# Kernel optimization log

Hardware: AMD Instinct MI355X
Metric: run time of the kernel (lower is better)

The kernel has to match this reference:

```python
import jax, jax.numpy as jnp
import numpy as np

QUANT_BITS = 8


def fake_quant(x, bits=QUANT_BITS):
    """Asymmetric signed per-tensor quantize->dequantize (GlobalMinMaxObserver)."""
    qmin = -(2 ** (bits - 1))
    qmax = 2 ** (bits - 1) - 1
    mn = jnp.minimum(jnp.min(x), 0.0)
    mx = jnp.maximum(jnp.max(x), 0.0)
    scale = jnp.maximum((mx - mn) / (qmax - qmin), 1e-8)
    zp = jnp.clip(jnp.round(qmin - mn / scale), qmin, qmax)
    q = jnp.clip(jnp.round(x / scale) + zp, qmin, qmax)
    return (q - zp) * scale


def hardsigmoid(x):
    return jnp.clip(x / 6.0 + 0.5, 0.0, 1.0)


def hardtanh(x):
    return jnp.clip(x, -1.0, 1.0)


def setup_inputs() -> dict:
    key = jax.random.key(0)
    ks = jax.random.split(key, 11)
    B, W, I, H = 16384, 32, 64, 64
    s = 1.0 / np.sqrt(I + H)
    return {
        "inputs": jax.random.normal(ks[0], (B, W, I), jnp.float32),
        "h_prev": jax.random.normal(ks[1], (B, W, H), jnp.float32),
        "c_prev": jax.random.normal(ks[2], (B, W, H), jnp.float32),
        "W_i": jax.random.normal(ks[3], (H, I + H), jnp.float32) * s,
        "b_i": jax.random.normal(ks[4], (H,), jnp.float32) * s,
        "W_f": jax.random.normal(ks[5], (H, I + H), jnp.float32) * s,
        "b_f": jax.random.normal(ks[6], (H,), jnp.float32) * s,
        "W_o": jax.random.normal(ks[7], (H, I + H), jnp.float32) * s,
        "b_o": jax.random.normal(ks[8], (H,), jnp.float32) * s,
        "W_c": jax.random.normal(ks[9], (H, I + H), jnp.float32) * s,
        "b_c": jax.random.normal(ks[10], (H,), jnp.float32) * s,
    }


def reference(inputs, h_prev, c_prev, W_i, b_i, W_f, b_f, W_o, b_o, W_c, b_c):
    # fake-quant every tensor as the module's QParams/observers do
    x = fake_quant(inputs)
    h = fake_quant(h_prev)
    c = fake_quant(c_prev)
    cat = fake_quant(jnp.concatenate([x, h], axis=-1))  # [B, W, I+H]

    def gate(Wg, bg):
        return fake_quant(jnp.einsum("bwk,hk->bwh", cat, fake_quant(Wg)) + fake_quant(bg))

    i_g = fake_quant(hardsigmoid(gate(W_i, b_i)))
    f_g = fake_quant(hardsigmoid(gate(W_f, b_f)))
    o_g = fake_quant(hardsigmoid(gate(W_o, b_o)))
    c_g = fake_quant(hardtanh(gate(W_c, b_c)))

    fc = fake_quant(f_g * c)
    ic = fake_quant(i_g * c_g)
    c_next = fake_quant(fc + ic)
    c_next_tanh = fake_quant(hardtanh(c_next))
    h_next = fake_quant(o_g * c_next_tanh)
    return h_next, c_next
```

## Files before the change

### kernel.cpp

```cpp
#include <hip/hip_runtime.h>
#include <stdint.h>

#define NE    33554432
#define MROWS 524288

typedef __attribute__((ext_vector_type(8))) short short8;
typedef __attribute__((ext_vector_type(4))) float f32x4;
typedef unsigned short ushort_t;
typedef unsigned char uchar_t;

__device__ __forceinline__ unsigned fenc(float f){
  unsigned u=__float_as_uint(f); return (u&0x80000000u)?~u:(u|0x80000000u);
}
__device__ __forceinline__ float fdec(unsigned u){
  return __uint_as_float((u&0x80000000u)?(u&0x7fffffffu):~u);
}
__device__ __forceinline__ void obs(float mn,float mx,float&s,float&zp){
  mn=fminf(mn,0.f); mx=fmaxf(mx,0.f);
  s=fmaxf((mx-mn)/255.0f,1e-8f);
  zp=fminf(fmaxf(rintf(-128.0f-mn/s),-128.f),127.f);
}
__device__ __forceinline__ float qof(float x,float s,float zp){
  return fminf(fmaxf(rintf(x/s)+zp,-128.f),127.f);
}
__device__ __forceinline__ float fqv(float x,float s,float zp){
  return (qof(x,s,zp)-zp)*s;
}
__device__ __forceinline__ void wred(float&mn,float&mx){
  #pragma unroll
  for(int o=32;o;o>>=1){mn=fminf(mn,__shfl_xor(mn,o));mx=fmaxf(mx,__shfl_xor(mx,o));}
}


__global__ void k0_init(unsigned* U){
  int t=threadIdx.x;
  if(t<11){U[2*t]=0xFFFFFFFFu;U[2*t+1]=0u;}
}

__global__ __launch_bounds__(256) void k1_minmax(const float* __restrict__ x,
    const float* __restrict__ h,const float* __restrict__ c,unsigned* U){
  __shared__ float red[8];
  int t=blockIdx.x*256+threadIdx.x, stride=gridDim.x*256;
  int w=threadIdx.x>>6,l=threadIdx.x&63;
  const float4* ps[3]={(const float4*)x,(const float4*)h,(const float4*)c};
  for(int q=0;q<3;q++){
    float mn=3.4e38f,mx=-3.4e38f;
    const float4* p=ps[q];
    for(int e=t;e<NE/4;e+=stride){
      float4 v=p[e];
      mn=fminf(mn,fminf(fminf(v.x,v.y),fminf(v.z,v.w)));
      mx=fmaxf(mx,fmaxf(fmaxf(v.x,v.y),fmaxf(v.z,v.w)));
    }
    wred(mn,mx);
    if(l==0){red[w]=mn;red[4+w]=mx;}
    __syncthreads();
    if(threadIdx.x==0){
      float bmn=fminf(fminf(red[0],red[1]),fminf(red[2],red[3]));
      float bmx=fmaxf(fmaxf(red[4],red[5]),fmaxf(red[6],red[7]));
      atomicMin(&U[2*q],fenc(bmn)); atomicMax(&U[2*q+1],fenc(bmx));
    }
    __syncthreads();
  }
}

__global__ __launch_bounds__(256) void k2_prep(const float* Wi,const float* bi,
    const float* Wf,const float* bfv,const float* Wo,const float* bo,
    const float* Wcg,const float* bcg,
    const unsigned* U,float* S,ushort_t* Wc,float* bq){
  __shared__ float smn[256],smx[256],sP[4];
  int t=threadIdx.x;
  if(t==0){
    float xmn=fdec(U[0]),xmx=fdec(U[1]),hmn=fdec(U[2]),hmx=fdec(U[3]),cmn=fdec(U[4]),cmx=fdec(U[5]);
    float sx,zx,sh,zh,sc,zc;
    obs(xmn,xmx,sx,zx);obs(hmn,hmx,sh,zh);obs(cmn,cmx,sc,zc);
    S[0]=sx;S[1]=zx;S[2]=sh;S[3]=zh;S[4]=sc;S[5]=zc;
    float cmn2=fminf(fqv(xmn,sx,zx),fqv(hmn,sh,zh));
    float cmx2=fmaxf(fqv(xmx,sx,zx),fqv(hmx,sh,zh));
    float scat,zcat;obs(cmn2,cmx2,scat,zcat);S[6]=scat;S[7]=zcat;
  }
  const float* Wp[4]={Wi,Wf,Wo,Wcg};
  const float* bp[4]={bi,bfv,bo,bcg};
  for(int g=0;g<4;g++){
    float mn=3.4e38f,mx=-3.4e38f;
    for(int i=t;i<8192;i+=256){float v=Wp[g][i];mn=fminf(mn,v);mx=fmaxf(mx,v);}
    smn[t]=mn;smx[t]=mx;__syncthreads();
    for(int ss=128;ss;ss>>=1){
      if(t<ss){smn[t]=fminf(smn[t],smn[t+ss]);smx[t]=fmaxf(smx[t],smx[t+ss]);}
      __syncthreads();
    }
    if(t==0){
      float s_,z_;obs(smn[0],smx[0],s_,z_);
      S[8+2*g]=s_;S[9+2*g]=z_;sP[0]=s_;sP[1]=z_;
      float bmn=3.4e38f,bmx=-3.4e38f;
      for(int i=0;i<64;i++){float v=bp[g][i];bmn=fminf(bmn,v);bmx=fmaxf(bmx,v);}
      float sb,zb;obs(bmn,bmx,sb,zb);sP[2]=sb;sP[3]=zb;
    }
    __syncthreads();
    float s_=sP[0],z_=sP[1],sb=sP[2],zb=sP[3];
    for(int i=t;i<8192;i+=256){
      float cv=qof(Wp[g][i],s_,z_)-z_;
      Wc[g*8192+i]=(ushort_t)(__float_as_uint(cv)>>16);
    }
    if(t<64) bq[g*64+t]=fqv(bp[g][t],sb,zb);
    __syncthreads();
  }
}

__global__ __launch_bounds__(256) void k3_quant(const float* __restrict__ x,
    const float* __restrict__ h,const float* __restrict__ c,
    const float* __restrict__ S,ushort_t* __restrict__ catc,uchar_t* __restrict__ qc){
  float sx=S[0],zx=S[1],sh=S[2],zh=S[3],sc=S[4],zc=S[5],scat=S[6],zcat=S[7];
  int t=blockIdx.x*256+threadIdx.x, stride=gridDim.x*256;
  const float4* xp=(const float4*)x; const float4* hp=(const float4*)h;
  for(int e=t;e<MROWS*32;e+=stride){
    int row=e>>5,k4=e&31;
    float4 v; float s1,z1;
    if(k4<16){v=xp[row*16+k4];s1=sx;z1=zx;}
    else     {v=hp[row*16+(k4-16)];s1=sh;z1=zh;}
    float c0=qof((qof(v.x,s1,z1)-z1)*s1,scat,zcat)-zcat;
    float c1=qof((qof(v.y,s1,z1)-z1)*s1,scat,zcat)-zcat;
    float c2=qof((qof(v.z,s1,z1)-z1)*s1,scat,zcat)-zcat;
    float c3=qof((qof(v.w,s1,z1)-z1)*s1,scat,zcat)-zcat;
    uint2 o;
    o.x=(__float_as_uint(c0)>>16)|((__float_as_uint(c1)>>16)<<16);
    o.y=(__float_as_uint(c2)>>16)|((__float_as_uint(c3)>>16)<<16);
    ((uint2*)catc)[e]=o;
  }
  const float4* cp=(const float4*)c;
  unsigned* qcp=(unsigned*)qc;
  for(int e=t;e<NE/4;e+=stride){
    float4 v=cp[e];
    int q0=(int)qof(v.x,sc,zc)+128,q1=(int)qof(v.y,sc,zc)+128;
    int q2=(int)qof(v.z,sc,zc)+128,q3=(int)qof(v.w,sc,zc)+128;
    qcp[e]=(unsigned)q0|((unsigned)q1<<8)|((unsigned)q2<<16)|((unsigned)q3<<24);
  }
}

__global__ __launch_bounds__(256) void g0_minmax(const ushort_t* __restrict__ catc,
    const ushort_t* __restrict__ Wc,const float* __restrict__ S,
    const float* __restrict__ bq,unsigned* U){
  int tid=threadIdx.x,w=tid>>6,l=tid&63,l15=l&15,lq=l>>4;
  float sgp=S[6]*S[8+2*w];
  short8 bf[4][4];
  #pragma unroll
  for(int nt=0;nt<4;nt++)
    #pragma unroll
    for(int ks=0;ks<4;ks++)
      bf[nt][ks]=*(const short8*)(Wc+w*8192+(nt*16+l15)*128+ks*32+lq*8);
  float bqr[4];
  #pragma unroll
  for(int nt=0;nt<4;nt++) bqr[nt]=bq[w*64+nt*16+l15];
  float mn=3.4e38f,mx=-3.4e38f;
  for(int gi=0;gi<8;gi++){
    int rowbase=(blockIdx.x*8+gi)*64;
    #pragma unroll
    for(int mt=0;mt<4;mt++){
      const ushort_t* arow=catc+(size_t)(rowbase+mt*16+l15)*128;
      short8 af[4];
      #pragma unroll
      for(int ks=0;ks<4;ks++) af[ks]=*(const short8*)(arow+ks*32+lq*8);
      f32x4 acc[4];
      #pragma unroll
      for(int nt=0;nt<4;nt++) acc[nt]=(f32x4){0.f,0.f,0.f,0.f};
      #pragma unroll
      for(int ks=0;ks<4;ks++)
        #pragma unroll
        for(int nt=0;nt<4;nt++)
          acc[nt]=__builtin_amdgcn_mfma_f32_16x16x32_bf16(af[ks],bf[nt][ks],acc[nt],0,0,0);
      #pragma unroll
      for(int nt=0;nt<4;nt++)
        #pragma unroll
        for(int r=0;r<4;r++){
          float v=sgp*acc[nt][r]+bqr[nt];
          mn=fminf(mn,v);mx=fmaxf(mx,v);
        }
    }
  }
  wred(mn,mx);
  if(l==0){atomicMin(&U[6+2*w],fenc(mn));atomicMax(&U[7+2*w],fenc(mx));}
}

__global__ __launch_bounds__(256,2) void g1_codes(const ushort_t* __restrict__ catc,
    const ushort_t* __restrict__ Wc,const float* __restrict__ S,
    const float* __restrict__ bq,const uchar_t* __restrict__ qc,
    const float* __restrict__ LUTa,unsigned* U,
    unsigned* __restrict__ qpack,uchar_t* __restrict__ qo){
  __shared__ float ldsq[4][64][64];
  __shared__ float lut[1024];
  __shared__ float red[16];
  int tid=threadIdx.x,w=tid>>6,l=tid&63,l15=l&15,lq=l>>4;
  for(int i=tid;i<1024;i+=256) lut[i]=LUTa[i];
  float sgp=S[6]*S[8+2*w];
  float sg1=S[16+2*w],zg1=S[17+2*w];
  float sc=S[4],zc128=S[5]+128.0f;
  short8 bf[4][4];
  #pragma unroll
  for(int nt=0;nt<4;nt++)
    #pragma unroll
    for(int ks=0;ks<4;ks++)
      bf[nt][ks]=*(const short8*)(Wc+w*8192+(nt*16+l15)*128+ks*32+lq*8);
  float bqr[4];
  #pragma unroll
  for(int nt=0;nt<4;nt++) bqr[nt]=bq[w*64+nt*16+l15];
  float fmn=3.4e38f,fmx=-3.4e38f,imn=3.4e38f,imx=-3.4e38f;
  for(int gi=0;gi<8;gi++){
    int grp=blockIdx.x*8+gi;
    int rowbase=grp*64;
    #pragma unroll
    for(int mt=0;mt<4;mt++){
      const ushort_t* arow=catc+(size_t)(rowbase+mt*16+l15)*128;
      short8 af[4];
      #pragma unroll
      for(int ks=0;ks<4;ks++) af[ks]=*(const short8*)(arow+ks*32+lq*8);
      f32x4 acc[4];
      #pragma unroll
      for(int nt=0;nt<4;nt++) acc[nt]=(f32x4){0.f,0.f,0.f,0.f};
      #pragma unroll
      for(int ks=0;ks<4;ks++)
        #pragma unroll
        for(int nt=0;nt<4;nt++)
          acc[nt]=__builtin_amdgcn_mfma_f32_16x16x32_bf16(af[ks],bf[nt][ks],acc[nt],0,0,0);
      #pragma unroll
      for(int nt=0;nt<4;nt++)
        #pragma unroll
        for(int r=0;r<4;r++){
          float v=sgp*acc[nt][r]+bqr[nt];
          ldsq[w][mt*16+lq*4+r][nt*16+l15]=qof(v,sg1,zg1);
        }
    }
    __syncthreads();
    #pragma unroll
    for(int i=0;i<16;i++){
      int e=tid+256*i;
      int row=e>>6,col=e&63;
      int gidx=grp*4096+e;
      int q0=(int)ldsq[0][row][col]+128;
      int q1=(int)ldsq[1][row][col]+128;
      int q2=(int)ldsq[2][row][col]+128;
      int q3=(int)ldsq[3][row][col]+128;
      int qcb=(int)qc[gidx];
      qpack[gidx]=(unsigned)q0|((unsigned)q1<<8)|((unsigned)q3<<16)|((unsigned)qcb<<24);
      qo[gidx]=(uchar_t)q2;
      float avi=lut[q0],avf=lut[256+q1],avcg=lut[768+q3];
      float cv=((float)qcb-zc128)*sc;
      float fc=avf*cv,ic=avi*avcg;
      fmn=fminf(fmn,fc);fmx=fmaxf(fmx,fc);
      imn=fminf(imn,ic);imx=fmaxf(imx,ic);
    }
    __syncthreads();
  }
  wred(fmn,fmx);wred(imn,imx);
  if(l==0){red[w]=fmn;red[4+w]=fmx;red[8+w]=imn;red[12+w]=imx;}
  __syncthreads();
  if(tid==0){
    float a=fminf(fminf(red[0],red[1]),fminf(red[2],red[3]));
    float b=fmaxf(fmaxf(red[4],red[5]),fmaxf(red[6],red[7]));
    atomicMin(&U[14],fenc(a));atomicMax(&U[15],fenc(b));
    a=fminf(fminf(red[8],red[9]),fminf(red[10],red[11]));
    b=fmaxf(fmaxf(red[12],red[13]),fmaxf(red[14],red[15]));
    atomicMin(&U[16],fenc(a));atomicMax(&U[17],fenc(b));
  }
}

__global__ __launch_bounds__(256) void e2_cn(const unsigned* __restrict__ qpack,
    const float* __restrict__ S,const float* __restrict__ LUTa,
    unsigned* U,ushort_t* __restrict__ qfcic){
  __shared__ float lut[1024];
  __shared__ float red[8];
  int tid=threadIdx.x;
  for(int i=tid;i<1024;i+=256) lut[i]=LUTa[i];
  float sc=S[4],zc128=S[5]+128.0f;
  float sfc=S[32],zfc=S[33],sic=S[34],zic=S[35];
  __syncthreads();
  float mn=3.4e38f,mx=-3.4e38f;
  int t=blockIdx.x*256+tid,stride=gridDim.x*256;
  for(int e=t;e<NE;e+=stride){
    unsigned u=qpack[e];
    int q0=u&255,q1=(u>>8)&255,q3=(u>>16)&255,qcb=u>>24;
    float avi=lut[q0],avf=lut[256+q1],avcg=lut[768+q3];
    float cv=((float)qcb-zc128)*sc;
    float fc=avf*cv,ic=avi*avcg;
    float qfc=qof(fc,sfc,zfc),qic=qof(ic,sic,zic);
    float cn=(qfc-zfc)*sfc+(qic-zic)*sic;
    mn=fminf(mn,cn);mx=fmaxf(mx,cn);
    qfcic[e]=(ushort_t)(((int)qfc+128)|(((int)qic+128)<<8));
  }
  int w=tid>>6,l=tid&63;
  wred(mn,mx);
  if(l==0){red[w]=mn;red[4+w]=mx;}
  __syncthreads();
  if(tid==0){
    float a=fminf(fminf(red[0],red[1]),fminf(red[2],red[3]));
    float b=fmaxf(fmaxf(red[4],red[5]),fmaxf(red[6],red[7]));
    atomicMin(&U[18],fenc(a));atomicMax(&U[19],fenc(b));
  }
}

__global__ __launch_bounds__(256) void e3_hmm(const ushort_t* __restrict__ qfcic,
    const uchar_t* __restrict__ qo,const float* __restrict__ S,
    const float* __restrict__ LUTa,const float* __restrict__ LUTct,
    unsigned* U,uchar_t* __restrict__ qcn){
  __shared__ float lao[256],lct[256];
  __shared__ float red[8];
  int tid=threadIdx.x;
  lao[tid]=LUTa[512+tid];lct[tid]=LUTct[tid];
  float sfc=S[32],zfc128=S[33]+128.0f,sic=S[34],zic128=S[35]+128.0f;
  float scn=S[36],zcn=S[37];
  __syncthreads();
  float mn=3.4e38f,mx=-3.4e38f;
  int t=blockIdx.x*256+tid,stride=gridDim.x*256;
  for(int e=t;e<NE;e+=stride){
    int u=qfcic[e];
    float fcv=((float)(u&255)-zfc128)*sfc;
    float icv=((float)(u>>8)-zic128)*sic;
    float cn=fcv+icv;
    float qcf=qof(cn,scn,zcn);
    int qb=(int)qcf+128;
    qcn[e]=(uchar_t)qb;
    float hr=lao[qo[e]]*lct[qb];
    mn=fminf(mn,hr);mx=fmaxf(mx,hr);
  }
  int w=tid>>6,l=tid&63;
  wred(mn,mx);
  if(l==0){red[w]=mn;red[4+w]=mx;}
  __syncthreads();
  if(tid==0){
    float a=fminf(fminf(red[0],red[1]),fminf(red[2],red[3]));
    float b=fmaxf(fmaxf(red[4],red[5]),fmaxf(red[6],red[7]));
    atomicMin(&U[20],fenc(a));atomicMax(&U[21],fenc(b));
  }
}

__global__ __launch_bounds__(256) void k_post(int stage,const unsigned* U,float* S,
    float* LUTa,float* LUTct){
  __shared__ float sh[16];
  int t=threadIdx.x;
  if(stage==0){
    if(t==0){
      for(int g=0;g<4;g++){
        float mn=fdec(U[6+2*g]),mx=fdec(U[7+2*g]);
        float s1,z1;obs(mn,mx,s1,z1);S[16+2*g]=s1;S[17+2*g]=z1;
        float gmn=fqv(mn,s1,z1),gmx=fqv(mx,s1,z1);
        float amn,amx;
        if(g==3){amn=fminf(fmaxf(gmn,-1.f),1.f);amx=fminf(fmaxf(gmx,-1.f),1.f);}
        else{amn=fminf(fmaxf(gmn/6.0f+0.5f,0.f),1.f);amx=fminf(fmaxf(gmx/6.0f+0.5f,0.f),1.f);}
        float s2,z2;obs(amn,amx,s2,z2);S[24+2*g]=s2;S[25+2*g]=z2;
        sh[4*g]=s1;sh[4*g+1]=z1;sh[4*g+2]=s2;sh[4*g+3]=z2;
      }
    }
    __syncthreads();
    for(int g=0;g<4;g++){
      float s1=sh[4*g],z1=sh[4*g+1],s2=sh[4*g+2],z2=sh[4*g+3];
      float g1=((float)(t-128)-z1)*s1;
      float a=(g==3)?fminf(fmaxf(g1,-1.f),1.f):fminf(fmaxf(g1/6.0f+0.5f,0.f),1.f);
      LUTa[g*256+t]=fqv(a,s2,z2);
    }
  } else if(stage==1){
    if(t==0){
      float s,z;
      obs(fdec(U[14]),fdec(U[15]),s,z);S[32]=s;S[33]=z;
      obs(fdec(U[16]),fdec(U[17]),s,z);S[34]=s;S[35]=z;
    }
  } else if(stage==2){
    if(t==0){
      float mn=fdec(U[18]),mx=fdec(U[19]);
      float s,z;obs(mn,mx,s,z);S[36]=s;S[37]=z;
      float tmn=fminf(fmaxf(fqv(mn,s,z),-1.f),1.f);
      float tmx=fminf(fmaxf(fqv(mx,s,z),-1.f),1.f);
      float s2,z2;obs(tmn,tmx,s2,z2);S[38]=s2;S[39]=z2;
      sh[0]=s;sh[1]=z;sh[2]=s2;sh[3]=z2;
    }
    __syncthreads();
    float scn=sh[0],zcn=sh[1],sct=sh[2],zct=sh[3];
    float cnv=((float)(t-128)-zcn)*scn;
    float ct=fminf(fmaxf(cnv,-1.f),1.f);
    LUTct[t]=fqv(ct,sct,zct);
  } else {
    if(t==0){float s,z;obs(fdec(U[20]),fdec(U[21]),s,z);S[40]=s;S[41]=z;}
  }
}

__global__ __launch_bounds__(256) void k9_out(const uchar_t* __restrict__ qo,
    const uchar_t* __restrict__ qcn,const float* __restrict__ S,
    const float* __restrict__ LUTa,const float* __restrict__ LUTct,
    float* __restrict__ hout,float* __restrict__ cout){
  __shared__ float lao[256],lct[256];
  int tid=threadIdx.x;
  lao[tid]=LUTa[512+tid];lct[tid]=LUTct[tid];
  float scn=S[36],zcn128=S[37]+128.0f,shn=S[40],zhn=S[41];
  __syncthreads();
  int t=blockIdx.x*256+tid,stride=gridDim.x*256;
  const unsigned* op=(const unsigned*)qo;
  const unsigned* cp=(const unsigned*)qcn;
  for(int e=t;e<NE/4;e+=stride){
    unsigned uo=op[e],uc=cp[e];
    float4 hv,cv;
    float* ph=&hv.x;float* pc=&cv.x;
    #pragma unroll
    for(int j=0;j<4;j++){
      int qoj=(uo>>(8*j))&255,qcj=(uc>>(8*j))&255;
      float cnv=((float)qcj-zcn128)*scn;
      float hr=lao[qoj]*lct[qcj];
      float qh=qof(hr,shn,zhn);
      ph[j]=(qh-zhn)*shn;
      pc[j]=cnv;
    }
    ((float4*)hout)[e]=hv;
    ((float4*)cout)[e]=cv;
  }
}

extern "C" void kernel_launch(void* const* d_in,const int* in_sizes,int n_in,
                              void* d_out,int out_size,void* d_ws,size_t ws_size,
                              hipStream_t stream){
  (void)in_sizes;(void)n_in;(void)out_size;(void)ws_size;
  const float* x  =(const float*)d_in[0];
  const float* h  =(const float*)d_in[1];
  const float* c  =(const float*)d_in[2];
  const float* Wi =(const float*)d_in[3];  const float* bi =(const float*)d_in[4];
  const float* Wf =(const float*)d_in[5];  const float* bfv=(const float*)d_in[6];
  const float* Wo =(const float*)d_in[7];  const float* bo =(const float*)d_in[8];
  const float* Wcg=(const float*)d_in[9];  const float* bcg=(const float*)d_in[10];

  char* ws=(char*)d_ws;
  unsigned* U =(unsigned*)ws;
  float* S    =(float*)(ws+128);
  float* bq   =(float*)(ws+512);
  ushort_t* Wc=(ushort_t*)(ws+2048);
  float* LUTa =(float*)(ws+69632);
  float* LUTct=(float*)(ws+73728);
  uchar_t* qc =(uchar_t*)(ws+(1<<20));
  uchar_t* qo =qc +(size_t)NE;
  uchar_t* qcn=qo +(size_t)NE;
  ushort_t* catc=(ushort_t*)d_out;
  unsigned* qpack=(unsigned*)((float*)d_out+NE);
  ushort_t* qfcic=(ushort_t*)d_out;
  float* h_out=(float*)d_out;
  float* c_out=(float*)d_out+NE;

  k0_init<<<1,64,0,stream>>>(U);
  k1_minmax<<<1024,256,0,stream>>>(x,h,c,U);
  k2_prep<<<1,256,0,stream>>>(Wi,bi,Wf,bfv,Wo,bo,Wcg,bcg,U,S,Wc,bq);
  k3_quant<<<2048,256,0,stream>>>(x,h,c,S,catc,qc);
  g0_minmax<<<1024,256,0,stream>>>(catc,Wc,S,bq,U);
  k_post<<<1,256,0,stream>>>(0,U,S,LUTa,LUTct);
  g1_codes<<<1024,256,0,stream>>>(catc,Wc,S,bq,qc,LUTa,U,qpack,qo);
  k_post<<<1,256,0,stream>>>(1,U,S,LUTa,LUTct);
  e2_cn<<<2048,256,0,stream>>>(qpack,S,LUTa,U,qfcic);
  k_post<<<1,256,0,stream>>>(2,U,S,LUTa,LUTct);
  e3_hmm<<<2048,256,0,stream>>>(qfcic,qo,S,LUTa,LUTct,U,qcn);
  k_post<<<1,256,0,stream>>>(3,U,S,LUTa,LUTct);
  k9_out<<<2048,256,0,stream>>>(qo,qcn,S,LUTa,LUTct,h_out,c_out);
}
```

Before: 1.286 ms.

## Remove post kernels, recompute scales in consumers, vectorize elementwise passes, retune grids

Removes the four single-block k_post launches; each consumer kernel now derives the observer scales and builds its activation LUTs from the atomic min/max words itself. The x/h to cat requantization becomes a small LUT built in k2_prep. g0 tracks raw accumulator min/max per column and applies the affine transform once at the end. g1 uses a half-size LDS tile to raise occupancy and writes packed uint4 stores, while e2 and e3 are vectorized to four elements per thread. Grid sizes and launch bounds are enlarged and k1 is unrolled by four. The cost is redundant per-block scale and LUT computation.

Measured after the change: 1.615 ms. 1.26x slower.

```diff
diff --git a/kernel.cpp b/kernel.cpp
--- a/kernel.cpp
+++ b/kernel.cpp
@@ -29,6 +29,27 @@
 __device__ __forceinline__ void wred(float&mn,float&mx){
   #pragma unroll
   for(int o=32;o;o>>=1){mn=fminf(mn,__shfl_xor(mn,o));mx=fmaxf(mx,__shfl_xor(mx,o));}
+}
+__device__ __forceinline__ void stage0(const unsigned* U,int g,float&s1,float&z1,float&s2,float&z2){
+  float mn=fdec(U[6+2*g]),mx=fdec(U[7+2*g]);
+  obs(mn,mx,s1,z1);
+  float gmn=fqv(mn,s1,z1),gmx=fqv(mx,s1,z1);
+  float amn,amx;
+  if(g==3){amn=fminf(fmaxf(gmn,-1.f),1.f);amx=fminf(fmaxf(gmx,-1.f),1.f);}
+  else{amn=fminf(fmaxf(gmn/6.0f+0.5f,0.f),1.f);amx=fminf(fmaxf(gmx/6.0f+0.5f,0.f),1.f);}
+  obs(amn,amx,s2,z2);
+}
+__device__ __forceinline__ float lut_entry(int t,int g,float s1,float z1,float s2,float z2){
+  float g1=((float)(t-128)-z1)*s1;
+  float a=(g==3)?fminf(fmaxf(g1,-1.f),1.f):fminf(fmaxf(g1/6.0f+0.5f,0.f),1.f);
+  return fqv(a,s2,z2);
+}
+__device__ __forceinline__ void stage2v(const unsigned* U,float&scn,float&zcn,float&sct,float&zct){
+  float mn=fdec(U[18]),mx=fdec(U[19]);
+  obs(mn,mx,scn,zcn);
+  float tmn=fminf(fmaxf(fqv(mn,scn,zcn),-1.f),1.f);
+  float tmx=fminf(fmaxf(fqv(mx,scn,zcn),-1.f),1.f);
+  obs(tmn,tmx,sct,zct);
 }
 
 
@@ -46,10 +67,16 @@
   for(int q=0;q<3;q++){
     float mn=3.4e38f,mx=-3.4e38f;
     const float4* p=ps[q];
-    for(int e=t;e<NE/4;e+=stride){
-      float4 v=p[e];
-      mn=fminf(mn,fminf(fminf(v.x,v.y),fminf(v.z,v.w)));
-      mx=fmaxf(mx,fmaxf(fmaxf(v.x,v.y),fmaxf(v.z,v.w)));
+    for(int e=t;e<NE/4;e+=4*stride){
+      float4 a=p[e],b=p[e+stride],c4=p[e+2*stride],d=p[e+3*stride];
+      mn=fminf(mn,fminf(fminf(a.x,a.y),fminf(a.z,a.w)));
+      mx=fmaxf(mx,fmaxf(fmaxf(a.x,a.y),fmaxf(a.z,a.w)));
+      mn=fminf(mn,fminf(fminf(b.x,b.y),fminf(b.z,b.w)));
+      mx=fmaxf(mx,fmaxf(fmaxf(b.x,b.y),fmaxf(b.z,b.w)));
+      mn=fminf(mn,fminf(fminf(c4.x,c4.y),fminf(c4.z,c4.w)));
+      mx=fmaxf(mx,fmaxf(fmaxf(c4.x,c4.y),fmaxf(c4.z,c4.w)));
+      mn=fminf(mn,fminf(fminf(d.x,d.y),fminf(d.z,d.w)));
+      mx=fmaxf(mx,fmaxf(fmaxf(d.x,d.y),fmaxf(d.z,d.w)));
     }
     wred(mn,mx);
     if(l==0){red[w]=mn;red[4+w]=mx;}
@@ -66,17 +93,27 @@
 __global__ __launch_bounds__(256) void k2_prep(const float* Wi,const float* bi,
     const float* Wf,const float* bfv,const float* Wo,const float* bo,
     const float* Wcg,const float* bcg,
-    const unsigned* U,float* S,ushort_t* Wc,float* bq){
-  __shared__ float smn[256],smx[256],sP[4];
+    const unsigned* U,float* S,ushort_t* Wc,float* bq,ushort_t* LUTcx){
+  __shared__ float smn[256],smx[256],sP[4],sS[8];
   int t=threadIdx.x;
   if(t==0){
     float xmn=fdec(U[0]),xmx=fdec(U[1]),hmn=fdec(U[2]),hmx=fdec(U[3]),cmn=fdec(U[4]),cmx=fdec(U[5]);
     float sx,zx,sh,zh,sc,zc;
     obs(xmn,xmx,sx,zx);obs(hmn,hmx,sh,zh);obs(cmn,cmx,sc,zc);
     S[0]=sx;S[1]=zx;S[2]=sh;S[3]=zh;S[4]=sc;S[5]=zc;
+    sS[0]=sx;sS[1]=zx;sS[2]=sh;sS[3]=zh;sS[4]=sc;sS[5]=zc;
     float cmn2=fminf(fqv(xmn,sx,zx),fqv(hmn,sh,zh));
     float cmx2=fmaxf(fqv(xmx,sx,zx),fqv(hmx,sh,zh));
     float scat,zcat;obs(cmn2,cmx2,scat,zcat);S[6]=scat;S[7]=zcat;
+    sS[6]=scat;sS[7]=zcat;
+  }
+  __syncthreads();
+  {
+    float sx=sS[0],zx=sS[1],sh=sS[2],zh=sS[3],scat=sS[6],zcat=sS[7];
+    float cx=qof(((float)(t-128)-zx)*sx,scat,zcat)-zcat;
+    float ch=qof(((float)(t-128)-zh)*sh,scat,zcat)-zcat;
+    LUTcx[t]    =(ushort_t)(__float_as_uint(cx)>>16);
+    LUTcx[256+t]=(ushort_t)(__float_as_uint(ch)>>16);
   }
   const float* Wp[4]={Wi,Wf,Wo,Wcg};
   const float* bp[4]={bi,bfv,bo,bcg};
@@ -108,22 +145,27 @@
 
 __global__ __launch_bounds__(256) void k3_quant(const float* __restrict__ x,
     const float* __restrict__ h,const float* __restrict__ c,
-    const float* __restrict__ S,ushort_t* __restrict__ catc,uchar_t* __restrict__ qc){
-  float sx=S[0],zx=S[1],sh=S[2],zh=S[3],sc=S[4],zc=S[5],scat=S[6],zcat=S[7];
-  int t=blockIdx.x*256+threadIdx.x, stride=gridDim.x*256;
+    const float* __restrict__ S,const ushort_t* __restrict__ LUTcx,
+    ushort_t* __restrict__ catc,uchar_t* __restrict__ qc){
+  __shared__ ushort_t lcx[512];
+  int tid=threadIdx.x;
+  for(int i=tid;i<512;i+=256) lcx[i]=LUTcx[i];
+  float sx=S[0],zx=S[1],sh=S[2],zh=S[3],sc=S[4],zc=S[5];
+  __syncthreads();
+  int t=blockIdx.x*256+tid, stride=gridDim.x*256;
   const float4* xp=(const float4*)x; const float4* hp=(const float4*)h;
   for(int e=t;e<MROWS*32;e+=stride){
     int row=e>>5,k4=e&31;
-    float4 v; float s1,z1;
-    if(k4<16){v=xp[row*16+k4];s1=sx;z1=zx;}
-    else     {v=hp[row*16+(k4-16)];s1=sh;z1=zh;}
-    float c0=qof((qof(v.x,s1,z1)-z1)*s1,scat,zcat)-zcat;
-    float c1=qof((qof(v.y,s1,z1)-z1)*s1,scat,zcat)-zcat;
-    float c2=qof((qof(v.z,s1,z1)-z1)*s1,scat,zcat)-zcat;
-    float c3=qof((qof(v.w,s1,z1)-z1)*s1,scat,zcat)-zcat;
+    float4 v; float s1,z1; int off;
+    if(k4<16){v=xp[row*16+k4];s1=sx;z1=zx;off=0;}
+    else     {v=hp[row*16+(k4-16)];s1=sh;z1=zh;off=256;}
+    int q0=(int)qof(v.x,s1,z1)+128;
+    int q1=(int)qof(v.y,s1,z1)+128;
+    int q2=(int)qof(v.z,s1,z1)+128;
+    int q3=(int)qof(v.w,s1,z1)+128;
     uint2 o;
-    o.x=(__float_as_uint(c0)>>16)|((__float_as_uint(c1)>>16)<<16);
-    o.y=(__float_as_uint(c2)>>16)|((__float_as_uint(c3)>>16)<<16);
+    o.x=(unsigned)lcx[off+q0]|((unsigned)lcx[off+q1]<<16);
+    o.y=(unsigned)lcx[off+q2]|((unsigned)lcx[off+q3]<<16);
     ((uint2*)catc)[e]=o;
   }
   const float4* cp=(const float4*)c;
@@ -136,7 +178,7 @@
   }
 }
 
-__global__ __launch_bounds__(256) void g0_minmax(const ushort_t* __restrict__ catc,
+__global__ __launch_bounds__(256,4) void g0_minmax(const ushort_t* __restrict__ catc,
     const ushort_t* __restrict__ Wc,const float* __restrict__ S,
     const float* __restrict__ bq,unsigned* U){
   int tid=threadIdx.x,w=tid>>6,l=tid&63,l15=l&15,lq=l>>4;
@@ -150,48 +192,57 @@
   float bqr[4];
   #pragma unroll
   for(int nt=0;nt<4;nt++) bqr[nt]=bq[w*64+nt*16+l15];
-  float mn=3.4e38f,mx=-3.4e38f;
-  for(int gi=0;gi<8;gi++){
-    int rowbase=(blockIdx.x*8+gi)*64;
-    #pragma unroll
-    for(int mt=0;mt<4;mt++){
-      const ushort_t* arow=catc+(size_t)(rowbase+mt*16+l15)*128;
-      short8 af[4];
-      #pragma unroll
-      for(int ks=0;ks<4;ks++) af[ks]=*(const short8*)(arow+ks*32+lq*8);
-      f32x4 acc[4];
-      #pragma unroll
-      for(int nt=0;nt<4;nt++) acc[nt]=(f32x4){0.f,0.f,0.f,0.f};
-      #pragma unroll
-      for(int ks=0;ks<4;ks++)
-        #pragma unroll
-        for(int nt=0;nt<4;nt++)
-          acc[nt]=__builtin_amdgcn_mfma_f32_16x16x32_bf16(af[ks],bf[nt][ks],acc[nt],0,0,0);
+  float mnA[4],mxA[4];
+  #pragma unroll
+  for(int nt=0;nt<4;nt++){mnA[nt]=3.4e38f;mxA[nt]=-3.4e38f;}
+  for(int u=0;u<8;u++){
+    int grp=blockIdx.x*2+(u>>2), mt=u&3;
+    const ushort_t* arow=catc+(size_t)(grp*64+mt*16+l15)*128;
+    short8 af[4];
+    #pragma unroll
+    for(int ks=0;ks<4;ks++) af[ks]=*(const short8*)(arow+ks*32+lq*8);
+    f32x4 acc[4];
+    #pragma unroll
+    for(int nt=0;nt<4;nt++) acc[nt]=(f32x4){0.f,0.f,0.f,0.f};
+    #pragma unroll
+    for(int ks=0;ks<4;ks++)
       #pragma unroll
       for(int nt=0;nt<4;nt++)
-        #pragma unroll
-        for(int r=0;r<4;r++){
-          float v=sgp*acc[nt][r]+bqr[nt];
-          mn=fminf(mn,v);mx=fmaxf(mx,v);
-        }
-    }
+        acc[nt]=__builtin_amdgcn_mfma_f32_16x16x32_bf16(af[ks],bf[nt][ks],acc[nt],0,0,0);
+    #pragma unroll
+    for(int nt=0;nt<4;nt++)
+      #pragma unroll
+      for(int r=0;r<4;r++){
+        mnA[nt]=fminf(mnA[nt],acc[nt][r]);
+        mxA[nt]=fmaxf(mxA[nt],acc[nt][r]);
+      }
+  }
+  float mn=3.4e38f,mx=-3.4e38f;
+  #pragma unroll
+  for(int nt=0;nt<4;nt++){
+    mn=fminf(mn,sgp*mnA[nt]+bqr[nt]);
+    mx=fmaxf(mx,sgp*mxA[nt]+bqr[nt]);
   }
   wred(mn,mx);
   if(l==0){atomicMin(&U[6+2*w],fenc(mn));atomicMax(&U[7+2*w],fenc(mx));}
 }
 
-__global__ __launch_bounds__(256,2) void g1_codes(const ushort_t* __restrict__ catc,
+__global__ __launch_bounds__(256,4) void g1_codes(const ushort_t* __restrict__ catc,
     const ushort_t* __restrict__ Wc,const float* __restrict__ S,
     const float* __restrict__ bq,const uchar_t* __restrict__ qc,
-    const float* __restrict__ LUTa,unsigned* U,
-    unsigned* __restrict__ qpack,uchar_t* __restrict__ qo){
-  __shared__ float ldsq[4][64][64];
+    unsigned* U,unsigned* __restrict__ qpack,uchar_t* __restrict__ qo){
+  __shared__ float ldsq[4][32][66];
   __shared__ float lut[1024];
   __shared__ float red[16];
   int tid=threadIdx.x,w=tid>>6,l=tid&63,l15=l&15,lq=l>>4;
-  for(int i=tid;i<1024;i+=256) lut[i]=LUTa[i];
+  float sg1,zg1;
+  #pragma unroll
+  for(int g=0;g<4;g++){
+    float s1,z1,s2,z2; stage0(U,g,s1,z1,s2,z2);
+    if(g==w){sg1=s1;zg1=z1;}
+    lut[g*256+tid]=lut_entry(tid,g,s1,z1,s2,z2);
+  }
   float sgp=S[6]*S[8+2*w];
-  float sg1=S[16+2*w],zg1=S[17+2*w];
   float sc=S[4],zc128=S[5]+128.0f;
   short8 bf[4][4];
   #pragma unroll
@@ -202,52 +253,61 @@
   float bqr[4];
   #pragma unroll
   for(int nt=0;nt<4;nt++) bqr[nt]=bq[w*64+nt*16+l15];
+  __syncthreads();
   float fmn=3.4e38f,fmx=-3.4e38f,imn=3.4e38f,imx=-3.4e38f;
-  for(int gi=0;gi<8;gi++){
-    int grp=blockIdx.x*8+gi;
-    int rowbase=grp*64;
-    #pragma unroll
-    for(int mt=0;mt<4;mt++){
-      const ushort_t* arow=catc+(size_t)(rowbase+mt*16+l15)*128;
-      short8 af[4];
+  for(int gi=0;gi<4;gi++){
+    int grp=blockIdx.x*4+gi;
+    #pragma unroll
+    for(int half=0;half<2;half++){
       #pragma unroll
-      for(int ks=0;ks<4;ks++) af[ks]=*(const short8*)(arow+ks*32+lq*8);
-      f32x4 acc[4];
-      #pragma unroll
-      for(int nt=0;nt<4;nt++) acc[nt]=(f32x4){0.f,0.f,0.f,0.f};
-      #pragma unroll
-      for(int ks=0;ks<4;ks++)
+      for(int mt2=0;mt2<2;mt2++){
+        int mt=half*2+mt2;
+        const ushort_t* arow=catc+(size_t)(grp*64+mt*16+l15)*128;
+        short8 af[4];
+        #pragma unroll
+        for(int ks=0;ks<4;ks++) af[ks]=*(const short8*)(arow+ks*32+lq*8);
+        f32x4 acc[4];
+        #pragma unroll
+        for(int nt=0;nt<4;nt++) acc[nt]=(f32x4){0.f,0.f,0.f,0.f};
+        #pragma unroll
+        for(int ks=0;ks<4;ks++)
+          #pragma unroll
+          for(int nt=0;nt<4;nt++)
+            acc[nt]=__builtin_amdgcn_mfma_f32_16x16x32_bf16(af[ks],bf[nt][ks],acc[nt],0,0,0);
         #pragma unroll
         for(int nt=0;nt<4;nt++)
-          acc[nt]=__builtin_amdgcn_mfma_f32_16x16x32_bf16(af[ks],bf[nt][ks],acc[nt],0,0,0);
+          #pragma unroll
+          for(int r=0;r<4;r++)
+            ldsq[w][mt2*16+lq*4+r][nt*16+l15]=qof(sgp*acc[nt][r]+bqr[nt],sg1,zg1);
+      }
+      __syncthreads();
       #pragma unroll
-      for(int nt=0;nt<4;nt++)
+      for(int it=0;it<2;it++){
+        int e4=(tid+it*256)<<2;
+        int gidx=grp*4096+half*2048+e4;
+        unsigned qcw=*(const unsigned*)(qc+gidx);
+        uint4 qp; unsigned qob=0;
         #pragma unroll
-        for(int r=0;r<4;r++){
-          float v=sgp*acc[nt][r]+bqr[nt];
-          ldsq[w][mt*16+lq*4+r][nt*16+l15]=qof(v,sg1,zg1);
+        for(int j=0;j<4;j++){
+          int row=(e4+j)>>6, col=(e4+j)&63;
+          int q0=(int)ldsq[0][row][col]+128;
+          int q1=(int)ldsq[1][row][col]+128;
+          int q2=(int)ldsq[2][row][col]+128;
+          int q3=(int)ldsq[3][row][col]+128;
+          int qcb=(int)((qcw>>(8*j))&255);
+          ((unsigned*)&qp)[j]=(unsigned)q0|((unsigned)q1<<8)|((unsigned)q3<<16)|((unsigned)qcb<<24);
+          qob|=(unsigned)q2<<(8*j);
+          float avi=lut[q0],avf=lut[256+q1],avcg=lut[768+q3];
+          float cv=((float)qcb-zc128)*sc;
+          float fc=avf*cv,ic=avi*avcg;
+          fmn=fminf(fmn,fc);fmx=fmaxf(fmx,fc);
+          imn=fminf(imn,ic);imx=fmaxf(imx,ic);
         }
-    }
-    __syncthreads();
-    #pragma unroll
-    for(int i=0;i<16;i++){
-      int e=tid+256*i;
-      int row=e>>6,col=e&63;
-      int gidx=grp*4096+e;
-      int q0=(int)ldsq[0][row][col]+128;
-      int q1=(int)ldsq[1][row][col]+128;
-      int q2=(int)ldsq[2][row][col]+128;
-      int q3=(int)ldsq[3][row][col]+128;
-      int qcb=(int)qc[gidx];
-      qpack[gidx]=(unsigned)q0|((unsigned)q1<<8)|((unsigned)q3<<16)|((unsigned)qcb<<24);
-      qo[gidx]=(uchar_t)q2;
-      float avi=lut[q0],avf=lut[256+q1],avcg=lut[768+q3];
-      float cv=((float)qcb-zc128)*sc;
-      float fc=avf*cv,ic=avi*avcg;
-      fmn=fminf(fmn,fc);fmx=fmaxf(fmx,fc);
-      imn=fminf(imn,ic);imx=fmaxf(imx,ic);
-    }
-    __syncthreads();
+        *(uint4*)(qpack+gidx)=qp;
+        *(unsigned*)(qo+gidx)=qob;
+      }
+      __syncthreads();
+    }
   }
   wred(fmn,fmx);wred(imn,imx);
   if(l==0){red[w]=fmn;red[4+w]=fmx;red[8+w]=imn;red[12+w]=imx;}
@@ -263,27 +323,42 @@
 }
 
 __global__ __launch_bounds__(256) void e2_cn(const unsigned* __restrict__ qpack,
-    const float* __restrict__ S,const float* __restrict__ LUTa,
-    unsigned* U,ushort_t* __restrict__ qfcic){
+    const float* __restrict__ S,unsigned* U,ushort_t* __restrict__ qfcic){
   __shared__ float lut[1024];
   __shared__ float red[8];
   int tid=threadIdx.x;
-  for(int i=tid;i<1024;i+=256) lut[i]=LUTa[i];
+  #pragma unroll
+  for(int g=0;g<4;g++){
+    float s1,z1,s2,z2; stage0(U,g,s1,z1,s2,z2);
+    lut[g*256+tid]=lut_entry(tid,g,s1,z1,s2,z2);
+  }
+  float sfc,zfc,sic,zic;
+  obs(fdec(U[14]),fdec(U[15]),sfc,zfc);
+  obs(fdec(U[16]),fdec(U[17]),sic,zic);
   float sc=S[4],zc128=S[5]+128.0f;
-  float sfc=S[32],zfc=S[33],sic=S[34],zic=S[35];
   __syncthreads();
   float mn=3.4e38f,mx=-3.4e38f;
   int t=blockIdx.x*256+tid,stride=gridDim.x*256;
-  for(int e=t;e<NE;e+=stride){
-    unsigned u=qpack[e];
-    int q0=u&255,q1=(u>>8)&255,q3=(u>>16)&255,qcb=u>>24;
-    float avi=lut[q0],avf=lut[256+q1],avcg=lut[768+q3];
-    float cv=((float)qcb-zc128)*sc;
-    float fc=avf*cv,ic=avi*avcg;
-    float qfc=qof(fc,sfc,zfc),qic=qof(ic,sic,zic);
-    float cn=(qfc-zfc)*sfc+(qic-zic)*sic;
-    mn=fminf(mn,cn);mx=fmaxf(mx,cn);
-    qfcic[e]=(ushort_t)(((int)qfc+128)|(((int)qic+128)<<8));
+  const uint4* qp4=(const uint4*)qpack;
+  uint2* qf2=(uint2*)qfcic;
+  for(int e=t;e<NE/4;e+=stride){
+    uint4 u4=qp4[e];
+    unsigned lo=0,hi=0;
+    #pragma unroll
+    for(int j=0;j<4;j++){
+      unsigned u=((const unsigned*)&u4)[j];
+      int q0=u&255,q1=(u>>8)&255,q3=(u>>16)&255,qcb=u>>24;
+      float avi=lut[q0],avf=lut[256+q1],avcg=lut[768+q3];
+      float cv=((float)qcb-zc128)*sc;
+      float fc=avf*cv,ic=avi*avcg;
+      float qfc=qof(fc,sfc,zfc),qic=qof(ic,sic,zic);
+      float cn=(qfc-zfc)*sfc+(qic-zic)*sic;
+      mn=fminf(mn,cn);mx=fmaxf(mx,cn);
+      unsigned pk=(unsigned)((int)qfc+128)|((unsigned)((int)qic+128)<<8);
+      if(j<2) lo|=pk<<(16*j); else hi|=pk<<(16*(j-2));
+    }
+    uint2 o; o.x=lo; o.y=hi;
+    qf2[e]=o;
   }
   int w=tid>>6,l=tid&63;
   wred(mn,mx);
@@ -297,28 +372,46 @@
 }
 
 __global__ __launch_bounds__(256) void e3_hmm(const ushort_t* __restrict__ qfcic,
-    const uchar_t* __restrict__ qo,const float* __restrict__ S,
-    const float* __restrict__ LUTa,const float* __restrict__ LUTct,
-    unsigned* U,uchar_t* __restrict__ qcn){
+    const uchar_t* __restrict__ qo,unsigned* U,uchar_t* __restrict__ qcn){
   __shared__ float lao[256],lct[256];
   __shared__ float red[8];
   int tid=threadIdx.x;
-  lao[tid]=LUTa[512+tid];lct[tid]=LUTct[tid];
-  float sfc=S[32],zfc128=S[33]+128.0f,sic=S[34],zic128=S[35]+128.0f;
-  float scn=S[36],zcn=S[37];
+  {
+    float s1,z1,s2,z2; stage0(U,2,s1,z1,s2,z2);
+    lao[tid]=lut_entry(tid,2,s1,z1,s2,z2);
+  }
+  float sfc,zfc,sic,zic;
+  obs(fdec(U[14]),fdec(U[15]),sfc,zfc);
+  obs(fdec(U[16]),fdec(U[17]),sic,zic);
+  float scn,zcn,sct,zct; stage2v(U,scn,zcn,sct,zct);
+  {
+    float cnv=((float)(tid-128)-zcn)*scn;
+    float ct=fminf(fmaxf(cnv,-1.f),1.f);
+    lct[tid]=fqv(ct,sct,zct);
+  }
+  float zfc128=zfc+128.0f,zic128=zic+128.0f;
   __syncthreads();
   float mn=3.4e38f,mx=-3.4e38f;
   int t=blockIdx.x*256+tid,stride=gridDim.x*256;
-  for(int e=t;e<NE;e+=stride){
-    int u=qfcic[e];
-    float fcv=((float)(u&255)-zfc128)*sfc;
-    float icv=((float)(u>>8)-zic128)*sic;
-    float cn=fcv+icv;
-    float qcf=qof(cn,scn,zcn);
-    int qb=(int)qcf+128;
-    qcn[e]=(uchar_t)qb;
-    float hr=lao[qo[e]]*lct[qb];
-    mn=fminf(mn,hr);mx=fmaxf(mx,hr);
+  const uint2* qf2=(const uint2*)qfcic;
+  const unsigned* qop=(const unsigned*)qo;
+  unsigned* qcp=(unsigned*)qcn;
+  for(int e=t;e<NE/4;e+=stride){
+    uint2 u=qf2[e]; unsigned uo=qop[e];
+    unsigned opk=0;
+    #pragma unroll
+    for(int j=0;j<4;j++){
+      unsigned pk=((j<2)?(u.x>>(16*j)):(u.y>>(16*(j-2))))&0xffffu;
+      float fcv=((float)(pk&255)-zfc128)*sfc;
+      float icv=((float)(pk>>8)-zic128)*sic;
+      float cn=fcv+icv;
+      float qcf=qof(cn,scn,zcn);
+      int qb=(int)qcf+128;
+      opk|=(unsigned)qb<<(8*j);
+      float hr=lao[(uo>>(8*j))&255]*lct[qb];
+      mn=fminf(mn,hr);mx=fmaxf(mx,hr);
+    }
+    qcp[e]=opk;
   }
   int w=tid>>6,l=tid&63;
   wred(mn,mx);
@@ -331,63 +424,23 @@
   }
 }
 
-__global__ __launch_bounds__(256) void k_post(int stage,const unsigned* U,float* S,
-    float* LUTa,float* LUTct){
-  __shared__ float sh[16];
-  int t=threadIdx.x;
-  if(stage==0){
-    if(t==0){
-      for(int g=0;g<4;g++){
-        float mn=fdec(U[6+2*g]),mx=fdec(U[7+2*g]);
-        float s1,z1;obs(mn,mx,s1,z1);S[16+2*g]=s1;S[17+2*g]=z1;
-        float gmn=fqv(mn,s1,z1),gmx=fqv(mx,s1,z1);
-        float amn,amx;
-        if(g==3){amn=fminf(fmaxf(gmn,-1.f),1.f);amx=fminf(fmaxf(gmx,-1.f),1.f);}
-        else{amn=fminf(fmaxf(gmn/6.0f+0.5f,0.f),1.f);amx=fminf(fmaxf(gmx/6.0f+0.5f,0.f),1.f);}
-        float s2,z2;obs(amn,amx,s2,z2);S[24+2*g]=s2;S[25+2*g]=z2;
-        sh[4*g]=s1;sh[4*g+1]=z1;sh[4*g+2]=s2;sh[4*g+3]=z2;
-      }
-    }
-    __syncthreads();
-    for(int g=0;g<4;g++){
-      float s1=sh[4*g],z1=sh[4*g+1],s2=sh[4*g+2],z2=sh[4*g+3];
-      float g1=((float)(t-128)-z1)*s1;
-      float a=(g==3)?fminf(fmaxf(g1,-1.f),1.f):fminf(fmaxf(g1/6.0f+0.5f,0.f),1.f);
-      LUTa[g*256+t]=fqv(a,s2,z2);
-    }
-  } else if(stage==1){
-    if(t==0){
-      float s,z;
-      obs(fdec(U[14]),fdec(U[15]),s,z);S[32]=s;S[33]=z;
-      obs(fdec(U[16]),fdec(U[17]),s,z);S[34]=s;S[35]=z;
-    }
-  } else if(stage==2){
-    if(t==0){
-      float mn=fdec(U[18]),mx=fdec(U[19]);
-      float s,z;obs(mn,mx,s,z);S[36]=s;S[37]=z;
-      float tmn=fminf(fmaxf(fqv(mn,s,z),-1.f),1.f);
-      float tmx=fminf(fmaxf(fqv(mx,s,z),-1.f),1.f);
-      float s2,z2;obs(tmn,tmx,s2,z2);S[38]=s2;S[39]=z2;
-      sh[0]=s;sh[1]=z;sh[2]=s2;sh[3]=z2;
-    }
-    __syncthreads();
-    float scn=sh[0],zcn=sh[1],sct=sh[2],zct=sh[3];
-    float cnv=((float)(t-128)-zcn)*scn;
-    float ct=fminf(fmaxf(cnv,-1.f),1.f);
-    LUTct[t]=fqv(ct,sct,zct);
-  } else {
-    if(t==0){float s,z;obs(fdec(U[20]),fdec(U[21]),s,z);S[40]=s;S[41]=z;}
-  }
-}
-
 __global__ __launch_bounds__(256) void k9_out(const uchar_t* __restrict__ qo,
-    const uchar_t* __restrict__ qcn,const float* __restrict__ S,
-    const float* __restrict__ LUTa,const float* __restrict__ LUTct,
+    const uchar_t* __restrict__ qcn,const unsigned* __restrict__ U,
     float* __restrict__ hout,float* __restrict__ cout){
   __shared__ float lao[256],lct[256];
   int tid=threadIdx.x;
-  lao[tid]=LUTa[512+tid];lct[tid]=LUTct[tid];
-  float scn=S[36],zcn128=S[37]+128.0f,shn=S[40],zhn=S[41];
+  {
+    float s1,z1,s2,z2; stage0(U,2,s1,z1,s2,z2);
+    lao[tid]=lut_entry(tid,2,s1,z1,s2,z2);
+  }
+  float scn,zcn,sct,zct; stage2v(U,scn,zcn,sct,zct);
+  {
+    float cnv=((float)(tid-128)-zcn)*scn;
+    float ct=fminf(fmaxf(cnv,-1.f),1.f);
+    lct[tid]=fqv(ct,sct,zct);
+  }
+  float shn,zhn; obs(fdec(U[20]),fdec(U[21]),shn,zhn);
+  float zcn128=zcn+128.0f;
   __syncthreads();
   int t=blockIdx.x*256+tid,stride=gridDim.x*256;
   const unsigned* op=(const unsigned*)qo;
@@ -426,9 +479,8 @@
   unsigned* U =(unsigned*)ws;
   float* S    =(float*)(ws+128);
   float* bq   =(float*)(ws+512);
-  ushort_t* Wc=(ushort_t*)(ws+2048);
-  float* LUTa =(float*)(ws+69632);
-  float* LUTct=(float*)(ws+73728);
+  ushort_t* LUTcx=(ushort_t*)(ws+1536);
+  ushort_t* Wc=(ushort_t*)(ws+4096);
   uchar_t* qc =(uchar_t*)(ws+(1<<20));
   uchar_t* qo =qc +(size_t)NE;
   uchar_t* qcn=qo +(size_t)NE;
@@ -439,16 +491,12 @@
   float* c_out=(float*)d_out+NE;
 
   k0_init<<<1,64,0,stream>>>(U);
-  k1_minmax<<<1024,256,0,stream>>>(x,h,c,U);
-  k2_prep<<<1,256,0,stream>>>(Wi,bi,Wf,bfv,Wo,bo,Wcg,bcg,U,S,Wc,bq);
-  k3_quant<<<2048,256,0,stream>>>(x,h,c,S,catc,qc);
-  g0_minmax<<<1024,256,0,stream>>>(catc,Wc,S,bq,U);
-  k_post<<<1,256,0,stream>>>(0,U,S,LUTa,LUTct);
-  g1_codes<<<1024,256,0,stream>>>(catc,Wc,S,bq,qc,LUTa,U,qpack,qo);
-  k_post<<<1,256,0,stream>>>(1,U,S,LUTa,LUTct);
-  e2_cn<<<2048,256,0,stream>>>(qpack,S,LUTa,U,qfcic);
-  k_post<<<1,256,0,stream>>>(2,U,S,LUTa,LUTct);
-  e3_hmm<<<2048,256,0,stream>>>(qfcic,qo,S,LUTa,LUTct,U,qcn);
-  k_post<<<1,256,0,stream>>>(3,U,S,LUTa,LUTct);
-  k9_out<<<2048,256,0,stream>>>(qo,qcn,S,LUTa,LUTct,h_out,c_out);
-}
+  k1_minmax<<<2048,256,0,stream>>>(x,h,c,U);
+  k2_prep<<<1,256,0,stream>>>(Wi,bi,Wf,bfv,Wo,bo,Wcg,bcg,U,S,Wc,bq,LUTcx);
+  k3_quant<<<4096,256,0,stream>>>(x,h,c,S,LUTcx,catc,qc);
+  g0_minmax<<<4096,256,0,stream>>>(catc,Wc,S,bq,U);
+  g1_codes<<<2048,256,0,stream>>>(catc,Wc,S,bq,qc,U,qpack,qo);
+  e2_cn<<<4096,256,0,stream>>>(qpack,S,U,qfcic);
+  e3_hmm<<<4096,256,0,stream>>>(qfcic,qo,U,qcn);
+  k9_out<<<4096,256,0,stream>>>(qo,qcn,U,h_out,c_out);
+}
```
